# Performance work log

Hardware: AMD Instinct MI355X
Metric: run time of the kernel (lower is better)

Reference implementation:

```python
import jax, jax.numpy as jnp
import numpy as np

N_HF = 128
N_RBF = 50
CUTOFF = 5.0
L = 3          # n_interactions
MAX_Z = 100
N_NODES = 30   # atoms per molecule
B = 1024       # molecules
N = B * N_NODES          # 30720 atoms
E = B * N_NODES * (N_NODES - 1)  # 890880 edges
N_REACT = 256
LOG2 = float(np.log(2.0))


def ssp(x):  # shifted softplus
    return jax.nn.softplus(x) - LOG2


def setup_inputs() -> dict:
    key = jax.random.key(0)
    ks = jax.random.split(key, 24)
    s = 0.02
    z = jax.random.randint(ks[0], (N,), 0, MAX_Z)
    coord = jax.random.normal(ks[1], (N, 3), jnp.float32) * 3.0
    # fully-connected edges within each molecule
    base = np.arange(N_NODES)
    row_l, col_l = np.meshgrid(base, base, indexing='ij')
    mask = row_l != col_l
    row_l, col_l = row_l[mask], col_l[mask]  # [n_nodes*(n_nodes-1)]
    offs = (np.arange(B) * N_NODES)[:, None]
    row = (offs + row_l[None, :]).reshape(-1)
    col = (offs + col_l[None, :]).reshape(-1)
    edge_index = jnp.asarray(np.stack([row, col]), jnp.int32)  # [2,E]
    atom_mask = jnp.ones((N, 1), jnp.float32)
    edge_mask = jnp.ones((E, 1), jnp.float32)
    reaction_indexes = jax.random.randint(ks[2], (B,), 0, N_REACT)
    reaction_indexes_signs = jnp.ones((B,), jnp.float32)
    # parameters
    emb = (jax.random.normal(ks[3], (MAX_Z, N_HF), jnp.float32)).at[0].set(0.0)  # padding_idx=0
    p = lambda k, shp: jax.random.normal(k, shp, jnp.float32) * s
    params = dict(
        in2f_W=p(ks[4], (L, N_HF, N_HF)),
        f_W1=p(ks[5], (L, N_RBF, N_HF)), f_b1=jnp.zeros((L, N_HF), jnp.float32),
        f_W2=p(ks[6], (L, N_HF, N_HF)), f_b2=jnp.zeros((L, N_HF), jnp.float32),
        o_W1=p(ks[7], (L, N_HF, N_HF)), o_b1=jnp.zeros((L, N_HF), jnp.float32),
        o_W2=p(ks[8], (L, N_HF, N_HF)), o_b2=jnp.zeros((L, N_HF), jnp.float32),
        dec_W1=p(ks[9], (N_HF, N_HF // 2)), dec_b1=jnp.zeros((N_HF // 2,), jnp.float32),
        dec_W2=p(ks[10], (N_HF // 2, 1)), dec_b2=jnp.zeros((1,), jnp.float32),
    )
    return dict(z=z, coord=coord, edge_index=edge_index, atom_mask=atom_mask,
                edge_mask=edge_mask, reaction_indexes=reaction_indexes,
                reaction_indexes_signs=reaction_indexes_signs, emb=emb,
                n_nodes=N_NODES, n_reactions=N_REACT, **params)


def reference(z, coord, edge_index, atom_mask, edge_mask, reaction_indexes,
              reaction_indexes_signs, emb, in2f_W, f_W1, f_b1, f_W2, f_b2,
              o_W1, o_b1, o_W2, o_b2, dec_W1, dec_b1, dec_W2, dec_b2,
              n_nodes, n_reactions):
    row, col = edge_index[0], edge_index[1]
    radial = jnp.linalg.norm(coord[row] - coord[col], axis=1)  # [E]
    h = emb[z]  # [N, n_hf]
    # GaussianRBF expansion
    offsets = jnp.linspace(0.0, CUTOFF, N_RBF)
    coeff = -0.5 / (offsets[1] - offsets[0]) ** 2
    rbf = jnp.exp(coeff * (radial[:, None] - offsets[None, :]) ** 2)  # [E, n_rbf]
    rbf = rbf * edge_mask
    # Cosine cutoff
    dc = 0.5 * (jnp.cos(radial * jnp.pi / CUTOFF) + 1.0) * (radial < CUTOFF)
    dist_cut = dc[:, None] * edge_mask  # [E,1]
    n_atoms = h.shape[0]
    for l in range(L):
        xf = h @ in2f_W[l]                                      # in2f (no bias)
        Wij = ssp(rbf @ f_W1[l] + f_b1[l]) @ f_W2[l] + f_b2[l]  # filter network
        Wij = Wij * dist_cut
        x_ij = xf[col] * Wij                                    # gather + multiply
        m = jax.ops.segment_sum(x_ij, row, num_segments=n_atoms)  # scatter-add
        m = ssp(m @ o_W1[l] + o_b1[l]) @ o_W2[l] + o_b2[l]      # f2out
        h = h + m
    h = h * atom_mask
    h = h.reshape(-1, n_nodes, N_HF).sum(axis=1)                # [B, n_hf]
    temp = ssp(h @ dec_W1 + dec_b1) @ dec_W2 + dec_b2           # [B, 1]
    pred = jnp.zeros((n_reactions,), jnp.float32).at[reaction_indexes].add(
        temp[:, 0] * reaction_indexes_signs)
    return pred
```

## Files before the change

kernel.cpp:

```cpp
#include <hip/hip_runtime.h>
#include <math.h>

#define NHF 128
#define NRBF 50
#define LAYERS 3
#define CUTOFF_F 5.0f
#define STEP_F (CUTOFF_F/49.0f)
#define LOG2_F 0.6931471805599453f
#define PI_F 3.14159265358979323846f
#define TBL 2048
#define TROWS (TBL+1)
#define TINV ((float)TBL / CUTOFF_F)

typedef __attribute__((ext_vector_type(8))) _Float16 fp16x8;
typedef __attribute__((ext_vector_type(4))) float f32x4;
typedef _Float16 f16x2 __attribute__((ext_vector_type(2)));

static __device__ __forceinline__ unsigned short f2h(float f){
    return __builtin_bit_cast(unsigned short, (_Float16)f);
}
static __device__ __forceinline__ unsigned packh(float lo, float hi){
    auto h = __builtin_amdgcn_cvt_pkrtz(lo, hi);
    return __builtin_bit_cast(unsigned, h);
}
static __device__ __forceinline__ float sspf(float x){
    return fmaxf(x, 0.0f) + log1pf(expf(-fabsf(x))) - LOG2_F;
}
static __device__ __forceinline__ float4 ld4(const float* p){ return *reinterpret_cast<const float4*>(p); }

__global__ __launch_bounds__(256) void k_pack(const float* __restrict__ in2f_W, const float* __restrict__ o_W1,
                                              const float* __restrict__ o_W2, uint4* __restrict__ Wp){
    int tid = blockIdx.x * 256 + threadIdx.x;
    if (tid >= 9 * 2048) return;
    int g = tid >> 11;
    int rem = tid & 2047;
    int s = rem >> 9;
    int f = (rem >> 6) & 7;
    int l = rem & 63;
    int layer = g / 3, type = g % 3;
    const float* src = (type == 0 ? in2f_W : (type == 1 ? o_W1 : o_W2)) + (size_t)layer * NHF * NHF;
    int row0 = s * 32 + ((l >> 4) << 3);
    int col  = (f << 4) + (l & 15);
    unsigned p0, p1, p2, p3;
    p0 = (unsigned)f2h(src[(row0+0)*NHF + col]) | ((unsigned)f2h(src[(row0+1)*NHF + col]) << 16);
    p1 = (unsigned)f2h(src[(row0+2)*NHF + col]) | ((unsigned)f2h(src[(row0+3)*NHF + col]) << 16);
    p2 = (unsigned)f2h(src[(row0+4)*NHF + col]) | ((unsigned)f2h(src[(row0+5)*NHF + col]) << 16);
    p3 = (unsigned)f2h(src[(row0+6)*NHF + col]) | ((unsigned)f2h(src[(row0+7)*NHF + col]) << 16);
    Wp[tid] = make_uint4(p0, p1, p2, p3);
}

__global__ __launch_bounds__(256) void k_table(const float* __restrict__ W1, const float* __restrict__ b1,
                                               const float* __restrict__ W2, const float* __restrict__ b2,
                                               unsigned short* __restrict__ Th){
    __shared__ float rbfL[2][4][52];
    __shared__ float hidL[2][4][128];
    int l = blockIdx.y;
    int tid = threadIdx.x;
    int g = tid >> 7, c = tid & 127;
    const float* W1l = W1 + (size_t)l * NRBF * NHF;
    const float* W2l = W2 + (size_t)l * NHF * NHF;
    int t0 = blockIdx.x * 8 + g * 4;
    const float coeff = -0.5f / (STEP_F * STEP_F);
    const float dr = CUTOFF_F / (float)TBL;
    if (c < NRBF){
        float off = c * STEP_F;
        #pragma unroll
        for (int i = 0; i < 4; i++){
            int t = t0 + i; if (t > TBL) t = TBL;
            float d = t * dr - off;
            rbfL[g][i][c] = expf(coeff * d * d);
        }
    }
    __syncthreads();
    float acc[4];
    float bc = b1[l * NHF + c];
    #pragma unroll
    for (int i = 0; i < 4; i++) acc[i] = bc;
    for (int j = 0; j < NRBF; j++){
        float wv = W1l[j * NHF + c];
        #pragma unroll
        for (int i = 0; i < 4; i++) acc[i] = fmaf(rbfL[g][i][j], wv, acc[i]);
    }
    #pragma unroll
    for (int i = 0; i < 4; i++) hidL[g][i][c] = sspf(acc[i]);
    __syncthreads();
    float b2c = b2[l * NHF + c];
    #pragma unroll
    for (int i = 0; i < 4; i++) acc[i] = b2c;
    for (int j = 0; j < NHF; j++){
        float wv = W2l[j * NHF + c];
        #pragma unroll
        for (int i = 0; i < 4; i++) acc[i] = fmaf(hidL[g][i][j], wv, acc[i]);
    }
    #pragma unroll
    for (int i = 0; i < 4; i++){
        int t = t0 + i; if (t > TBL) t = TBL;
        float r = t * dr;
        float dc = (t >= TBL) ? 0.0f : 0.5f * (cosf(r * (PI_F / CUTOFF_F)) + 1.0f);
        float v = acc[i] * dc;
        Th[((size_t)l * TROWS + t) * NHF + c] = __builtin_bit_cast(unsigned short, (_Float16)v);
    }
}

static __device__ __forceinline__ fp16x8 ldX(const unsigned* A_u, int rfbase, int ks, int l){
    int row = rfbase + (l & 15);
    int wc = ks * 16 + ((l >> 4) << 2);
    uint4 v = *reinterpret_cast<const uint4*>(&A_u[row * 64 + (wc ^ ((row & 7) << 2))]);
    return __builtin_bit_cast(fp16x8, v);
}
static __device__ __forceinline__ fp16x8 ldW(const uint4* __restrict__ Wp, int g, int ks, int cfg, int l){
    uint4 v = Wp[(((g << 2) + ks) * 8 + cfg) * 64 + l];
    return __builtin_bit_cast(fp16x8, v);
}

template<int EPI>
static __device__ __forceinline__ void gemm_phase(const uint4* __restrict__ Wp, int g,
                                                  const unsigned* A_u, uint2* D2,
                                                  float hreg[2][2][4], const float* __restrict__ bias,
                                                  int w, int l){
    f32x4 acc00 = {0,0,0,0}, acc01 = {0,0,0,0}, acc10 = {0,0,0,0}, acc11 = {0,0,0,0};
    #pragma unroll
    for (int ks = 0; ks < 4; ks++){
        fp16x8 wa0 = ldW(Wp, g, ks, w * 2 + 0, l);
        fp16x8 wa1 = ldW(Wp, g, ks, w * 2 + 1, l);
        fp16x8 xb0 = ldX(A_u, 0, ks, l);
        fp16x8 xb1 = ldX(A_u, 16, ks, l);
        acc00 = __builtin_amdgcn_mfma_f32_16x16x32_f16(wa0, xb0, acc00, 0, 0, 0);
        acc01 = __builtin_amdgcn_mfma_f32_16x16x32_f16(wa0, xb1, acc01, 0, 0, 0);
        acc10 = __builtin_amdgcn_mfma_f32_16x16x32_f16(wa1, xb0, acc10, 0, 0, 0);
        acc11 = __builtin_amdgcn_mfma_f32_16x16x32_f16(wa1, xb1, acc11, 0, 0, 0);
    }
    #pragma unroll
    for (int chf = 0; chf < 2; chf++){
        int ch0 = (w * 2 + chf) * 16 + ((l >> 4) << 2);
        float4 bv = {0,0,0,0};
        if (EPI >= 1) bv = ld4(bias + ch0);
        #pragma unroll
        for (int af = 0; af < 2; af++){
            f32x4 a = (chf == 0) ? (af == 0 ? acc00 : acc01) : (af == 0 ? acc10 : acc11);
            int atom = af * 16 + (l & 15);
            float v0 = a[0] + bv.x, v1 = a[1] + bv.y, v2 = a[2] + bv.z, v3 = a[3] + bv.w;
            if (EPI == 1){ v0 = sspf(v0); v1 = sspf(v1); v2 = sspf(v2); v3 = sspf(v3); }
            if (EPI == 2){
                v0 += hreg[chf][af][0]; hreg[chf][af][0] = v0;
                v1 += hreg[chf][af][1]; hreg[chf][af][1] = v1;
                v2 += hreg[chf][af][2]; hreg[chf][af][2] = v2;
                v3 += hreg[chf][af][3]; hreg[chf][af][3] = v3;
            }
            D2[(atom << 5) + (((ch0 >> 2) ^ ((atom & 7) << 1)))] = make_uint2(packh(v0, v1), packh(v2, v3));
        }
    }
}

__global__ __launch_bounds__(256, 4) void k_mega(const int* __restrict__ z, const float* __restrict__ coord,
                                                 const float* __restrict__ emask, const float* __restrict__ amask,
                                                 const float* __restrict__ emb,
                                                 const uint4* __restrict__ Wp,
                                                 const float* __restrict__ o_b1, const float* __restrict__ o_b2,
                                                 const unsigned* __restrict__ Tb,
                                                 const float* __restrict__ dW1, const float* __restrict__ db1,
                                                 const float* __restrict__ dW2, const float* __restrict__ db2,
                                                 const int* __restrict__ ridx, const float* __restrict__ rsign,
                                                 float* __restrict__ pred, int nn){
    __shared__ __align__(16) unsigned hbf[32 * 64];
    __shared__ __align__(16) unsigned xfb[32 * 64];
    __shared__ __align__(16) unsigned mbu[32 * 64];
    __shared__ int      pkE[32 * 32];
    __shared__ int      cntL[32];
    __shared__ int      cntP[16];
    __shared__ int      zL[32];
    __shared__ unsigned maskL[32];
    __shared__ float    cxyz[96];
    __shared__ float    amL[32];
    __shared__ float    hsb[NHF];

    int mol = blockIdx.x;
    int tid = threadIdx.x;
    int w = tid >> 6, l = tid & 63;
    int molA = mol * nn;
    int km = nn - 1;
    int ne = nn * km;

    uint2* hbf2 = reinterpret_cast<uint2*>(hbf);
    uint2* xfb2 = reinterpret_cast<uint2*>(xfb);
    uint2* mbu2 = reinterpret_cast<uint2*>(mbu);

    if (tid < 32){ maskL[tid] = 0u; cntL[tid] = 0; }
    if (tid < 3 * nn) cxyz[tid] = coord[(size_t)molA * 3 + tid];
    if (tid < 32)     amL[tid] = (tid < nn) ? amask[molA + tid] : 0.0f;
    if (tid < 32)     zL[tid]  = (tid < nn) ? z[molA + tid] : 0;
    __syncthreads();
    for (int e = tid; e < ne; e += 256){
        if (emask[(size_t)molA * km + e] != 0.0f){
            int a = e / km, k = e - a * km;
            atomicOr(&maskL[a], 1u << k);
        }
    }

    float hreg[2][2][4];
    #pragma unroll
    for (int chf = 0; chf < 2; chf++){
        int ch0 = (w * 2 + chf) * 16 + ((l >> 4) << 2);
        #pragma unroll
        for (int af = 0; af < 2; af++){
            int atom = af * 16 + (l & 15);
            float4 v = {0,0,0,0};
            if (atom < nn) v = ld4(emb + (size_t)zL[atom] * NHF + ch0);
            hreg[chf][af][0] = v.x; hreg[chf][af][1] = v.y;
            hreg[chf][af][2] = v.z; hreg[chf][af][3] = v.w;
            hbf2[(atom << 5) + (((ch0 >> 2) ^ ((atom & 7) << 1)))] = make_uint2(packh(v.x, v.y), packh(v.z, v.w));
        }
    }
    __syncthreads();

    if (tid < nn){
        int ai = tid;
        unsigned msk = maskL[ai];
        float ax = cxyz[ai*3], ay = cxyz[ai*3+1], az = cxyz[ai*3+2];
        int cnt = 0;
        for (int k = 0; k < km; k++){
            int nb = k + (k >= ai ? 1 : 0);
            float dx = ax - cxyz[nb*3], dy = ay - cxyz[nb*3+1], dz = az - cxyz[nb*3+2];
            float r = sqrtf(dx*dx + dy*dy + dz*dz);
            int t = (int)(r * TINV + 0.5f);
            if (((msk >> k) & 1u) && t < TBL){
                pkE[ai * 32 + cnt] = nb | (t << 8);
                cnt++;
            }
        }
        cntL[ai] = cnt;
    }
    __syncthreads();
    if (tid < 32){
        int mycnt = cntL[tid];
        int ocnt  = cntL[tid ^ 1];
        int mx = ((mycnt > ocnt ? mycnt : ocnt) + 3) & ~3;
        for (int k = mycnt; k < mx; k++) pkE[tid * 32 + k] = (TBL << 8);
        if (!(tid & 1)) cntP[tid >> 1] = mx;
    }
    __syncthreads();

    int h2 = l >> 5;
    int l5 = l & 31;
    for (int L = 0; L < LAYERS; L++){
        gemm_phase<0>(Wp, L * 3 + 0, hbf, xfb2, hreg, o_b1, w, l);
        __syncthreads();
        const char* TlB = (const char*)(Tb + (size_t)L * TROWS * 64);
        for (int pr = w; pr < 16; pr += 4){
            int a0 = 2 * pr + h2;
            int cnt = cntP[pr];
            const int* pe = &pkE[a0 * 32];
            f16x2 acc0; acc0[0] = (_Float16)0; acc0[1] = (_Float16)0;
            f16x2 acc1 = acc0;
            for (int k = 0; k < cnt; k += 4){
                #pragma unroll
                for (int j = 0; j < 4; j++){
                    int p = pe[k + j];
                    uint2 tw = *reinterpret_cast<const uint2*>(TlB + (p & ~0xFF) + (l5 << 3));
                    int atom = p & 31;
                    uint2 xw = xfb2[(atom << 5) + (l5 ^ ((atom & 7) << 1))];
                    f16x2 t0 = __builtin_bit_cast(f16x2, tw.x);
                    f16x2 t1 = __builtin_bit_cast(f16x2, tw.y);
                    f16x2 x0 = __builtin_bit_cast(f16x2, xw.x);
                    f16x2 x1 = __builtin_bit_cast(f16x2, xw.y);
                    acc0 = t0 * x0 + acc0;
                    acc1 = t1 * x1 + acc1;
                }
            }
            mbu2[(a0 << 5) + (l5 ^ ((a0 & 7) << 1))] =
                make_uint2(__builtin_bit_cast(unsigned, acc0), __builtin_bit_cast(unsigned, acc1));
        }
        __syncthreads();
        gemm_phase<1>(Wp, L * 3 + 1, mbu, xfb2, hreg, o_b1 + L * NHF, w, l);
        __syncthreads();
        gemm_phase<2>(Wp, L * 3 + 2, xfb, hbf2, hreg, o_b2 + L * NHF, w, l);
        __syncthreads();
    }

    {
        float s[2][4];
        #pragma unroll
        for (int chf = 0; chf < 2; chf++)
            #pragma unroll
            for (int r = 0; r < 4; r++)
                s[chf][r] = hreg[chf][0][r] * amL[l & 15] + hreg[chf][1][r] * amL[16 + (l & 15)];
        #pragma unroll
        for (int o = 1; o < 16; o <<= 1){
            #pragma unroll
            for (int chf = 0; chf < 2; chf++)
                #pragma unroll
                for (int r = 0; r < 4; r++)
                    s[chf][r] += __shfl_xor(s[chf][r], o);
        }
        if (!(l & 15)){
            #pragma unroll
            for (int chf = 0; chf < 2; chf++)
                #pragma unroll
                for (int r = 0; r < 4; r++)
                    hsb[(w * 2 + chf) * 16 + ((l >> 4) << 2) + r] = s[chf][r];
        }
    }
    __syncthreads();
    {
        float* red = (float*)pkE;
        int o = tid & 63, part = tid >> 6;
        float u = 0.0f;
        #pragma unroll 8
        for (int c = part * 32; c < part * 32 + 32; c++)
            u = fmaf(hsb[c], dW1[c * 64 + o], u);
        red[part * 64 + o] = u;
    }
    __syncthreads();
    if (tid < 64){
        float u = ((float*)pkE)[tid] + ((float*)pkE)[64 + tid] + ((float*)pkE)[128 + tid]
                + ((float*)pkE)[192 + tid] + db1[tid];
        float p = sspf(u) * dW2[tid];
        #pragma unroll
        for (int o = 32; o > 0; o >>= 1) p += __shfl_down(p, o);
        if (tid == 0) atomicAdd(&pred[ridx[mol]], (p + db2[0]) * rsign[mol]);
    }
}

extern "C" void kernel_launch(void* const* d_in, const int* in_sizes, int n_in,
                              void* d_out, int out_size, void* d_ws, size_t ws_size,
                              hipStream_t stream){
    const int*   z      = (const int*)  d_in[0];
    const float* coord  = (const float*)d_in[1];
    const float* amask  = (const float*)d_in[3];
    const float* emask  = (const float*)d_in[4];
    const int*   ridx   = (const int*)  d_in[5];
    const float* rsign  = (const float*)d_in[6];
    const float* emb    = (const float*)d_in[7];
    const float* in2f_W = (const float*)d_in[10];
    const float* f_W1   = (const float*)d_in[11];
    const float* f_b1   = (const float*)d_in[12];
    const float* f_W2   = (const float*)d_in[13];
    const float* f_b2   = (const float*)d_in[14];
    const float* o_W1   = (const float*)d_in[15];
    const float* o_b1   = (const float*)d_in[16];
    const float* o_W2   = (const float*)d_in[17];
    const float* o_b2   = (const float*)d_in[18];
    const float* dW1    = (const float*)d_in[19];
    const float* db1    = (const float*)d_in[20];
    const float* dW2    = (const float*)d_in[21];
    const float* db2    = (const float*)d_in[22];

    const int N  = in_sizes[0];
    const int B  = in_sizes[5];
    const int nn = N / B;
    (void)n_in; (void)ws_size;

    uint4*    Wp = (uint4*)d_ws;
    unsigned* Tb = (unsigned*)((char*)d_ws + 9 * 2048 * 16);

    (void)hipMemsetAsync(d_out, 0, (size_t)out_size * sizeof(float), stream);
    k_pack <<<72, 256, 0, stream>>>(in2f_W, o_W1, o_W2, Wp);
    k_table<<<dim3((TROWS + 7) / 8, LAYERS), 256, 0, stream>>>(f_W1, f_b1, f_W2, f_b2,
                                                               (unsigned short*)Tb);
    k_mega <<<B, 256, 0, stream>>>(z, coord, emask, amask, emb, Wp, o_b1, o_b2, Tb,
                                   dW1, db1, dW2, db2, ridx, rsign, (float*)d_out, nn);
}
```

Measured before the change: 105.5 us.

## Accumulate messages in fp32 with 16-byte loads, finer table, deterministic reaction reduce

The filter lookup table grows to twice as many rows. The message gather-multiply now has each lane handle 8 channels with 16-byte table and feature loads, accumulating in fp32 instead of packed fp16, with edge padding reduced to groups of four atoms. Softplus and RBF switch to exp2/log2 forms, and packh uses round-to-nearest conversion instead of cvt_pkrtz. The final reaction scatter replaces the atomics and memset with a separate per-reaction reduction kernel, which adds a launch and a serial scan over molecules. These changes mostly improve accuracy and determinism, with uncertain effect on speed.

```diff
diff --git a/kernel.cpp b/kernel.cpp
--- a/kernel.cpp
+++ b/kernel.cpp
@@ -8,7 +8,7 @@
 #define STEP_F (CUTOFF_F/49.0f)
 #define LOG2_F 0.6931471805599453f
 #define PI_F 3.14159265358979323846f
-#define TBL 2048
+#define TBL 4096
 #define TROWS (TBL+1)
 #define TINV ((float)TBL / CUTOFF_F)
 
@@ -20,11 +20,11 @@
     return __builtin_bit_cast(unsigned short, (_Float16)f);
 }
 static __device__ __forceinline__ unsigned packh(float lo, float hi){
-    auto h = __builtin_amdgcn_cvt_pkrtz(lo, hi);
-    return __builtin_bit_cast(unsigned, h);
+    return (unsigned)f2h(lo) | ((unsigned)f2h(hi) << 16);
 }
 static __device__ __forceinline__ float sspf(float x){
-    return fmaxf(x, 0.0f) + log1pf(expf(-fabsf(x))) - LOG2_F;
+    float t = exp2f(-fabsf(x) * 1.44269504f);
+    return fmaxf(x, 0.0f) + 0.69314718f * (log2f(1.0f + t) - 1.0f);
 }
 static __device__ __forceinline__ float4 ld4(const float* p){ return *reinterpret_cast<const float4*>(p); }
 
@@ -60,7 +60,7 @@
     const float* W1l = W1 + (size_t)l * NRBF * NHF;
     const float* W2l = W2 + (size_t)l * NHF * NHF;
     int t0 = blockIdx.x * 8 + g * 4;
-    const float coeff = -0.5f / (STEP_F * STEP_F);
+    const float coeff = -0.5f / (STEP_F * STEP_F) * 1.44269504f;
     const float dr = CUTOFF_F / (float)TBL;
     if (c < NRBF){
         float off = c * STEP_F;
@@ -68,7 +68,7 @@
         for (int i = 0; i < 4; i++){
             int t = t0 + i; if (t > TBL) t = TBL;
             float d = t * dr - off;
-            rbfL[g][i][c] = expf(coeff * d * d);
+            rbfL[g][i][c] = exp2f(coeff * d * d);
         }
     }
     __syncthreads();
@@ -98,7 +98,7 @@
         float r = t * dr;
         float dc = (t >= TBL) ? 0.0f : 0.5f * (cosf(r * (PI_F / CUTOFF_F)) + 1.0f);
         float v = acc[i] * dc;
-        Th[((size_t)l * TROWS + t) * NHF + c] = __builtin_bit_cast(unsigned short, (_Float16)v);
+        Th[((size_t)l * TROWS + t) * NHF + c] = f2h(v);
     }
 }
 
@@ -160,14 +160,13 @@
                                                  const unsigned* __restrict__ Tb,
                                                  const float* __restrict__ dW1, const float* __restrict__ db1,
                                                  const float* __restrict__ dW2, const float* __restrict__ db2,
-                                                 const int* __restrict__ ridx, const float* __restrict__ rsign,
-                                                 float* __restrict__ pred, int nn){
+                                                 float* __restrict__ tempv, int nn){
     __shared__ __align__(16) unsigned hbf[32 * 64];
     __shared__ __align__(16) unsigned xfb[32 * 64];
     __shared__ __align__(16) unsigned mbu[32 * 64];
     __shared__ int      pkE[32 * 32];
     __shared__ int      cntL[32];
-    __shared__ int      cntP[16];
+    __shared__ int      cntQ[8];
     __shared__ int      zL[32];
     __shared__ unsigned maskL[32];
     __shared__ float    cxyz[96];
@@ -183,7 +182,6 @@
 
     uint2* hbf2 = reinterpret_cast<uint2*>(hbf);
     uint2* xfb2 = reinterpret_cast<uint2*>(xfb);
-    uint2* mbu2 = reinterpret_cast<uint2*>(mbu);
 
     if (tid < 32){ maskL[tid] = 0u; cntL[tid] = 0; }
     if (tid < 3 * nn) cxyz[tid] = coord[(size_t)molA * 3 + tid];
@@ -232,43 +230,49 @@
     }
     __syncthreads();
     if (tid < 32){
-        int mycnt = cntL[tid];
-        int ocnt  = cntL[tid ^ 1];
-        int mx = ((mycnt > ocnt ? mycnt : ocnt) + 3) & ~3;
-        for (int k = mycnt; k < mx; k++) pkE[tid * 32 + k] = (TBL << 8);
-        if (!(tid & 1)) cntP[tid >> 1] = mx;
-    }
-    __syncthreads();
-
-    int h2 = l >> 5;
-    int l5 = l & 31;
+        int b4 = tid & ~3;
+        int m0 = cntL[b4], m1 = cntL[b4+1], m2 = cntL[b4+2], m3 = cntL[b4+3];
+        int mx = max(max(m0, m1), max(m2, m3));
+        mx = (mx + 1) & ~1;
+        for (int k = cntL[tid]; k < mx; k++) pkE[tid * 32 + k] = (TBL << 8);
+        if (!(tid & 3)) cntQ[tid >> 2] = mx;
+    }
+    __syncthreads();
+
+    int j16 = l & 15, g16 = l >> 4;
     for (int L = 0; L < LAYERS; L++){
         gemm_phase<0>(Wp, L * 3 + 0, hbf, xfb2, hreg, o_b1, w, l);
         __syncthreads();
-        const char* TlB = (const char*)(Tb + (size_t)L * TROWS * 64);
-        for (int pr = w; pr < 16; pr += 4){
-            int a0 = 2 * pr + h2;
-            int cnt = cntP[pr];
-            const int* pe = &pkE[a0 * 32];
-            f16x2 acc0; acc0[0] = (_Float16)0; acc0[1] = (_Float16)0;
-            f16x2 acc1 = acc0;
-            for (int k = 0; k < cnt; k += 4){
+        const char* Tlj = (const char*)(Tb + (size_t)L * TROWS * 64) + (j16 << 4);
+        for (int q = w; q < 8; q += 4){
+            int a = (q << 2) + g16;
+            int cnt = cntQ[q];
+            const int* pe = &pkE[a * 32];
+            float accf[8] = {0,0,0,0,0,0,0,0};
+            for (int k = 0; k < cnt; k += 2){
                 #pragma unroll
-                for (int j = 0; j < 4; j++){
-                    int p = pe[k + j];
-                    uint2 tw = *reinterpret_cast<const uint2*>(TlB + (p & ~0xFF) + (l5 << 3));
-                    int atom = p & 31;
-                    uint2 xw = xfb2[(atom << 5) + (l5 ^ ((atom & 7) << 1))];
-                    f16x2 t0 = __builtin_bit_cast(f16x2, tw.x);
-                    f16x2 t1 = __builtin_bit_cast(f16x2, tw.y);
-                    f16x2 x0 = __builtin_bit_cast(f16x2, xw.x);
-                    f16x2 x1 = __builtin_bit_cast(f16x2, xw.y);
-                    acc0 = t0 * x0 + acc0;
-                    acc1 = t1 * x1 + acc1;
+                for (int jj = 0; jj < 2; jj++){
+                    int p = pe[k + jj];
+                    uint4 tw = *reinterpret_cast<const uint4*>(Tlj + (p & ~0xFF));
+                    int ca = p & 31;
+                    uint4 xw = *reinterpret_cast<const uint4*>(&xfb[(ca << 6) + ((j16 ^ (ca & 7)) << 2)]);
+                    f16x2 t0 = __builtin_bit_cast(f16x2, tw.x), t1 = __builtin_bit_cast(f16x2, tw.y);
+                    f16x2 t2 = __builtin_bit_cast(f16x2, tw.z), t3 = __builtin_bit_cast(f16x2, tw.w);
+                    f16x2 x0 = __builtin_bit_cast(f16x2, xw.x), x1 = __builtin_bit_cast(f16x2, xw.y);
+                    f16x2 x2 = __builtin_bit_cast(f16x2, xw.z), x3 = __builtin_bit_cast(f16x2, xw.w);
+                    accf[0] += (float)t0[0] * (float)x0[0];
+                    accf[1] += (float)t0[1] * (float)x0[1];
+                    accf[2] += (float)t1[0] * (float)x1[0];
+                    accf[3] += (float)t1[1] * (float)x1[1];
+                    accf[4] += (float)t2[0] * (float)x2[0];
+                    accf[5] += (float)t2[1] * (float)x2[1];
+                    accf[6] += (float)t3[0] * (float)x3[0];
+                    accf[7] += (float)t3[1] * (float)x3[1];
                 }
             }
-            mbu2[(a0 << 5) + (l5 ^ ((a0 & 7) << 1))] =
-                make_uint2(__builtin_bit_cast(unsigned, acc0), __builtin_bit_cast(unsigned, acc1));
+            *reinterpret_cast<uint4*>(&mbu[(a << 6) + ((j16 ^ (a & 7)) << 2)]) =
+                make_uint4(packh(accf[0], accf[1]), packh(accf[2], accf[3]),
+                           packh(accf[4], accf[5]), packh(accf[6], accf[7]));
         }
         __syncthreads();
         gemm_phase<1>(Wp, L * 3 + 1, mbu, xfb2, hreg, o_b1 + L * NHF, w, l);
@@ -317,8 +321,28 @@
         float p = sspf(u) * dW2[tid];
         #pragma unroll
         for (int o = 32; o > 0; o >>= 1) p += __shfl_down(p, o);
-        if (tid == 0) atomicAdd(&pred[ridx[mol]], (p + db2[0]) * rsign[mol]);
-    }
+        if (tid == 0) tempv[mol] = p + db2[0];
+    }
+}
+
+__global__ __launch_bounds__(256) void k_pred(const float* __restrict__ tempv, const int* __restrict__ ridx,
+                                              const float* __restrict__ rsign, float* __restrict__ pred,
+                                              int nmol, int nreact){
+    extern __shared__ float sh[];
+    float* tv = sh;
+    int*   ri = (int*)(sh + nmol);
+    int tid = threadIdx.x;
+    for (int i = tid; i < nmol; i += 256){
+        tv[i] = tempv[i] * rsign[i];
+        ri[i] = ridx[i];
+    }
+    __syncthreads();
+    int r = blockIdx.x * 256 + tid;
+    if (r >= nreact) return;
+    float s = 0.0f;
+    for (int i = 0; i < nmol; i++)
+        if (ri[i] == r) s += tv[i];
+    pred[r] = s;
 }
 
 extern "C" void kernel_launch(void* const* d_in, const int* in_sizes, int n_in,
@@ -350,13 +374,15 @@
     const int nn = N / B;
     (void)n_in; (void)ws_size;
 
-    uint4*    Wp = (uint4*)d_ws;
-    unsigned* Tb = (unsigned*)((char*)d_ws + 9 * 2048 * 16);
-
-    (void)hipMemsetAsync(d_out, 0, (size_t)out_size * sizeof(float), stream);
+    uint4*    Wp    = (uint4*)d_ws;
+    unsigned* Tb    = (unsigned*)((char*)d_ws + 9 * 2048 * 16);
+    float*    tempv = (float*)((char*)Tb + (size_t)LAYERS * TROWS * 256);
+
     k_pack <<<72, 256, 0, stream>>>(in2f_W, o_W1, o_W2, Wp);
     k_table<<<dim3((TROWS + 7) / 8, LAYERS), 256, 0, stream>>>(f_W1, f_b1, f_W2, f_b2,
                                                                (unsigned short*)Tb);
     k_mega <<<B, 256, 0, stream>>>(z, coord, emask, amask, emb, Wp, o_b1, o_b2, Tb,
-                                   dW1, db1, dW2, db2, ridx, rsign, (float*)d_out, nn);
-}
+                                   dW1, db1, dW2, db2, tempv, nn);
+    k_pred <<<(out_size + 255) / 256, 256, B * 8, stream>>>(tempv, ridx, rsign,
+                                                            (float*)d_out, B, out_size);
+}
```

Result: slower. 144.1 us (+36.6%).
